# Performance work log

Measured on AMD Instinct MI355X. Metric: run time of the kernel, lower is better.

Reference implementation:

```python
import jax, jax.numpy as jnp
import numpy as np

D = 1024        # inputsize / d_model
G = 8           # groupnum (KV groups)
H = 16          # heads per group
DQ = 128        # qk head dim
DV = 128        # v head dim
FF = 1024       # ffoutsize
B, S = 1, 1024


def _rmsnorm(t, gamma, d_model):
    # torch F.normalize(x, dim=-1) * sqrt(d_model) * gamma
    n = jnp.sqrt(jnp.sum(t * t, axis=-1, keepdims=True))
    return t / jnp.maximum(n, 1e-12) * (d_model ** 0.5) * gamma


def setup_inputs() -> dict:
    key = jax.random.key(0)
    ks = jax.random.split(key, 8)
    std = 0.02
    x = jax.random.normal(ks[0], (B, S, D), dtype=jnp.float32)
    gamma_in = jnp.ones((D,), jnp.float32)
    Wq_w = jax.random.normal(ks[1], (H * G * DQ, D), jnp.float32) * std
    Wq_b = jnp.zeros((H * G * DQ,), jnp.float32)
    Wkv_w = jax.random.normal(ks[2], (G * (DQ + DV), D), jnp.float32) * std
    Wkv_b = jnp.zeros((G * (DQ + DV),), jnp.float32)
    gamma_z = jnp.ones((G * H * DV,), jnp.float32)
    W1 = jax.random.normal(ks[3], (FF * 2, G * H * DV), jnp.float32) * std
    b1 = jnp.zeros((FF * 2,), jnp.float32)
    W2 = jax.random.normal(ks[4], (FF, FF * 2), jnp.float32) * std
    b2 = jnp.zeros((FF,), jnp.float32)
    return {"x": x, "gamma_in": gamma_in, "Wq_w": Wq_w, "Wq_b": Wq_b,
            "Wkv_w": Wkv_w, "Wkv_b": Wkv_b, "gamma_z": gamma_z,
            "W1": W1, "b1": b1, "W2": W2, "b2": b2}


def reference(x, gamma_in, Wq_w, Wq_b, Wkv_w, Wkv_b, gamma_z, W1, b1, W2, b2):
    x = _rmsnorm(x, gamma_in, D)                      # (B,S,D)
    # self-attention path (m is None -> m = x)
    q = (x @ Wq_w.T + Wq_b).reshape(B, S, G, H, DQ)   # (B,S,G,H,dq)
    kv = x @ Wkv_w.T + Wkv_b                          # (B,S,G*(dq+dv))
    k, v = jnp.split(kv, 2, axis=-1)
    k = k.reshape(B, S, G, DQ)                        # (B,S,G,dq)
    v = v.reshape(B, S, G, DV)                        # (B,S,G,dv)
    scale = 1.0 / (DQ ** 0.5)
    scores = jnp.einsum('bsghd,bTgd->bghsT', q, k) * scale  # (B,G,H,S,S)
    attn = jax.nn.softmax(scores, axis=-1)
    z = jnp.einsum('bghsT,bTgd->bsghd', attn, v)      # (B,S,G,H,dv)
    z = z.reshape(B, S, G * H * DV)
    z = _rmsnorm(z, gamma_z, G * H * DV)
    h1 = jax.nn.silu(z @ W1.T + b1)                   # (B,S,2*FF)
    out = jax.nn.silu(h1 @ W2.T + b2)                 # (B,S,FF)
    return out
```

## Files before the change

### kernel.cpp

```cpp
#include <hip/hip_runtime.h>
#include <hip/hip_bf16.h>
#include <math.h>

typedef __attribute__((ext_vector_type(8))) short short8;
typedef __attribute__((ext_vector_type(4))) float floatx4;

__device__ __forceinline__ ushort f2bf(float f) {
  __hip_bfloat16 h = __float2bfloat16(f);
  return *reinterpret_cast<ushort*>(&h);
}
__device__ __forceinline__ float bf2f(ushort u) {
  union { unsigned int i; float f; } c; c.i = ((unsigned)u) << 16; return c.f;
}

__device__ __forceinline__ void lds_dma16(const void* g, void* l) {
  __builtin_amdgcn_global_load_lds((const __attribute__((address_space(1))) void*)g,
                                   (__attribute__((address_space(3))) void*)l, 16, 0, 0);
}

__global__ __launch_bounds__(256) void cvt_all(const float* __restrict__ p0, ushort* __restrict__ o0, int b0,
                                               const float* __restrict__ p1, ushort* __restrict__ o1, int b1,
                                               const float* __restrict__ p2, ushort* __restrict__ o2, int b2,
                                               const float* __restrict__ p3, ushort* __restrict__ o3) {
  int b = blockIdx.x;
  const float* in; ushort* out; int base;
  if (b < b0)            { in = p0; out = o0; base = 0; }
  else if (b < b0 + b1)  { in = p1; out = o1; base = b0; }
  else if (b < b0 + b1 + b2) { in = p2; out = o2; base = b0 + b1; }
  else                   { in = p3; out = o3; base = b0 + b1 + b2; }
  int i = (b - base) * 256 + threadIdx.x;
  float4 v = ((const float4*)in)[i];
  ushort4 o;
  o.x = f2bf(v.x); o.y = f2bf(v.y); o.z = f2bf(v.z); o.w = f2bf(v.w);
  ((ushort4*)out)[i] = o;
}

__global__ __launch_bounds__(256) void rmsnorm_f32(const float* __restrict__ x,
                                                   const float* __restrict__ gamma,
                                                   ushort* __restrict__ y, int D, float sqrtD) {
  const int row = blockIdx.x;
  const float* xr = x + (size_t)row * D;
  float ss = 0.f;
  for (int i = threadIdx.x * 4; i < D; i += 1024) {
    float4 v = *(const float4*)&xr[i];
    ss += v.x * v.x + v.y * v.y + v.z * v.z + v.w * v.w;
  }
#pragma unroll
  for (int off = 1; off < 64; off <<= 1) ss += __shfl_xor(ss, off);
  __shared__ float red[4];
  if ((threadIdx.x & 63) == 0) red[threadIdx.x >> 6] = ss;
  __syncthreads();
  ss = red[0] + red[1] + red[2] + red[3];
  const float sc = sqrtD / fmaxf(sqrtf(ss), 1e-12f);
  for (int i = threadIdx.x * 4; i < D; i += 1024) {
    float4 v = *(const float4*)&xr[i];
    ushort4 o;
    o.x = f2bf(v.x * sc * gamma[i]);
    o.y = f2bf(v.y * sc * gamma[i + 1]);
    o.z = f2bf(v.z * sc * gamma[i + 2]);
    o.w = f2bf(v.w * sc * gamma[i + 3]);
    *(ushort4*)&y[(size_t)row * D + i] = o;
  }
}

__global__ __launch_bounds__(256) void rmsnorm_bf16(const ushort* __restrict__ x,
                                                    const float* __restrict__ gamma,
                                                    ushort* __restrict__ y, int D, float sqrtD) {
  const int row = blockIdx.x;
  const ushort* xr = x + (size_t)row * D;
  float ss = 0.f;
  for (int i = threadIdx.x * 8; i < D; i += 2048) {
    short8 v = *(const short8*)&xr[i];
#pragma unroll
    for (int e = 0; e < 8; e++) { float f = bf2f((ushort)v[e]); ss += f * f; }
  }
#pragma unroll
  for (int off = 1; off < 64; off <<= 1) ss += __shfl_xor(ss, off);
  __shared__ float red[4];
  if ((threadIdx.x & 63) == 0) red[threadIdx.x >> 6] = ss;
  __syncthreads();
  ss = red[0] + red[1] + red[2] + red[3];
  const float sc = sqrtD / fmaxf(sqrtf(ss), 1e-12f);
  for (int i = threadIdx.x * 8; i < D; i += 2048) {
    short8 v = *(const short8*)&xr[i];
    short8 ov;
#pragma unroll
    for (int e = 0; e < 8; e++) ov[e] = (short)f2bf(bf2f((ushort)v[e]) * sc * gamma[i + e]);
    *(short8*)&y[(size_t)row * D + i] = ov;
  }
}

template <int EPI, int ACT, int OUTBF16>
__global__ __launch_bounds__(256, 3) void gemm3(const ushort* __restrict__ A,
                                                const ushort* __restrict__ B,
                                                const float* __restrict__ bias,
                                                const float* __restrict__ bias2,
                                                void* __restrict__ C1,
                                                void* __restrict__ C2,
                                                int M, int N, int K, int Ksplit, float scale) {
  __shared__ ushort As[128 * 64];
  __shared__ ushort Bs[128 * 64];
  const int tid = threadIdx.x;
  const int wave = tid >> 6;
  const int lane = tid & 63;
  const int c16 = lane & 15;
  const int quad = lane >> 4;
  const int wm = wave >> 1;
  const int wn = wave & 1;
  const size_t m0 = (size_t)blockIdx.x * 128;
  const size_t n0 = (size_t)blockIdx.y * 128;
  const int kbeg = blockIdx.z * Ksplit;
  const int kend = kbeg + Ksplit;

  const int rsub = lane >> 3;
  const int csw = (lane & 7) ^ rsub;

  const floatx4 zero = {0.f, 0.f, 0.f, 0.f};
  floatx4 acc[4][4];
#pragma unroll
  for (int a = 0; a < 4; a++)
#pragma unroll
    for (int b = 0; b < 4; b++) acc[a][b] = zero;

  for (int k0 = kbeg; k0 < kend; k0 += 64) {
    __syncthreads();
#pragma unroll
    for (int i = 0; i < 4; i++) {
      const int j = wave * 4 + i;
      const int r = j * 8 + rsub;
      lds_dma16(&A[(m0 + r) * K + k0 + csw * 8], (void*)(As + j * 512));
      lds_dma16(&B[(n0 + r) * K + k0 + csw * 8], (void*)(Bs + j * 512));
    }
    __syncthreads();
#pragma unroll
    for (int kc = 0; kc < 2; kc++) {
      short8 af[4], bf4[4];
#pragma unroll
      for (int mt = 0; mt < 4; mt++) {
        const int row = wm * 64 + mt * 16 + c16;
        af[mt] = *(const short8*)&As[row * 64 + (((kc * 4 + quad) ^ (row & 7)) << 3)];
      }
#pragma unroll
      for (int nt = 0; nt < 4; nt++) {
        const int row = wn * 64 + nt * 16 + c16;
        bf4[nt] = *(const short8*)&Bs[row * 64 + (((kc * 4 + quad) ^ (row & 7)) << 3)];
      }
#pragma unroll
      for (int mt = 0; mt < 4; mt++)
#pragma unroll
        for (int nt = 0; nt < 4; nt++)
          acc[mt][nt] = __builtin_amdgcn_mfma_f32_16x16x32_bf16(af[mt], bf4[nt], acc[mt][nt], 0, 0, 0);
    }
  }

#pragma unroll
  for (int mt = 0; mt < 4; mt++) {
#pragma unroll
    for (int nt = 0; nt < 4; nt++) {
      const size_t col = n0 + wn * 64 + nt * 16 + c16;
      const size_t row0 = m0 + wm * 64 + mt * 16 + quad * 4;
      if (EPI == 0) {
        const float bv = bias[col];
#pragma unroll
        for (int r = 0; r < 4; r++) {
          float v = acc[mt][nt][r] + bv;
          if (ACT) v = v / (1.f + __expf(-v));
          if (OUTBF16) ((ushort*)C1)[(row0 + r) * N + col] = f2bf(v);
          else         ((float*)C1)[(row0 + r) * N + col] = v;
        }
      } else if (EPI == 1) {
        float* plane = (float*)C1 + (size_t)blockIdx.z * M * N;
#pragma unroll
        for (int r = 0; r < 4; r++)
          plane[(row0 + r) * N + col] = acc[mt][nt][r];
      } else {
        if (col < 16384) {
          const float bv = bias[col];
#pragma unroll
          for (int r = 0; r < 4; r++)
            ((ushort*)C1)[(row0 + r) * 16384 + col] = f2bf((acc[mt][nt][r] + bv) * scale);
        } else {
          const size_t ckv = col - 16384;
          const float bv = bias2[ckv];
#pragma unroll
          for (int r = 0; r < 4; r++)
            ((ushort*)C2)[(row0 + r) * 2048 + ckv] = f2bf(acc[mt][nt][r] + bv);
        }
      }
    }
  }
}

template <int NZ, int OUTBF16>
__global__ __launch_bounds__(256) void epi_sum_silu(const float* __restrict__ accb,
                                                    const float* __restrict__ bias,
                                                    void* __restrict__ outp, int N, int n4,
                                                    size_t plane4) {
  int i = blockIdx.x * 256 + threadIdx.x;
  if (i >= n4) return;
  float4 v = ((const float4*)accb)[i];
#pragma unroll
  for (int z = 1; z < NZ; z++) {
    float4 p = ((const float4*)accb)[i + z * plane4];
    v.x += p.x; v.y += p.y; v.z += p.z; v.w += p.w;
  }
  const float4 b = *(const float4*)&bias[(i * 4) % N];
  v.x += b.x; v.y += b.y; v.z += b.z; v.w += b.w;
  v.x = v.x / (1.f + __expf(-v.x));
  v.y = v.y / (1.f + __expf(-v.y));
  v.z = v.z / (1.f + __expf(-v.z));
  v.w = v.w / (1.f + __expf(-v.w));
  if (OUTBF16) {
    ushort4 o; o.x = f2bf(v.x); o.y = f2bf(v.y); o.z = f2bf(v.z); o.w = f2bf(v.w);
    ((ushort4*)outp)[i] = o;
  } else {
    ((float4*)outp)[i] = v;
  }
}

__global__ __launch_bounds__(256) void vtrans(const ushort* __restrict__ KV,
                                              ushort* __restrict__ VT) {
  __shared__ ushort Vl[64 * 138];
  const int tid = threadIdx.x;
  const int t0 = blockIdx.x * 64;
  const int g = blockIdx.y;
#pragma unroll
  for (int i = 0; i < 16; i++) {
    int idx = tid + i * 256;
    int r = idx >> 6, dc = idx & 63;
    *(uint*)&Vl[r * 138 + dc * 2] =
        *(const uint*)&KV[(size_t)(t0 + r) * 2048 + 1024 + g * 128 + dc * 2];
  }
  __syncthreads();
#pragma unroll
  for (int i = 0; i < 4; i++) {
    int idx = tid + i * 256;
    int dv = idx >> 3, tch = idx & 7;
    short8 o;
#pragma unroll
    for (int j = 0; j < 8; j++) o[j] = (short)Vl[(tch * 8 + j) * 138 + dv];
    *(short8*)&VT[(size_t)g * 131072 + (size_t)dv * 1024 + t0 + tch * 8] = o;
  }
}

__global__ __launch_bounds__(256, 2) void attn4(const ushort* __restrict__ Q,
                                                const ushort* __restrict__ KV,
                                                const ushort* __restrict__ VT,
                                                ushort* __restrict__ Z) {
  constexpr int SEQ = 1024;
  __shared__ ushort Kl[64 * 132];
  __shared__ ushort Vt[128 * 68];
  __shared__ ushort Pl[4 * 64 * 68];
  const int tid = threadIdx.x;
  const int wave = tid >> 6;
  const int lane = tid & 63;
  const int c16 = lane & 15;
  const int quad = lane >> 4;
  const int hh = blockIdx.y;
  const int g = hh >> 4;
  const int qbase = blockIdx.x * 256 + wave * 64;
  ushort* Pw = Pl + wave * 64 * 68;

  short8 aq[4][4];
#pragma unroll
  for (int mt = 0; mt < 4; mt++)
#pragma unroll
    for (int kc = 0; kc < 4; kc++)
      aq[mt][kc] = *(const short8*)&Q[(size_t)(qbase + mt * 16 + c16) * 16384 + hh * 128 + kc * 32 + quad * 8];

  const floatx4 zero = {0.f, 0.f, 0.f, 0.f};
  floatx4 o[4][8];
  float lacc[4][4];
#pragma unroll
  for (int mt = 0; mt < 4; mt++) {
#pragma unroll
    for (int nt = 0; nt < 8; nt++) o[mt][nt] = zero;
#pragma unroll
    for (int r = 0; r < 4; r++) lacc[mt][r] = 0.f;
  }

  const ushort* Kg = KV + (size_t)g * 128;
  const ushort* Vg = VT + (size_t)g * 131072;

  for (int t0 = 0; t0 < SEQ; t0 += 64) {
    __syncthreads();
#pragma unroll
    for (int i = 0; i < 4; i++) {
      int idx = tid + i * 256;
      int r = idx >> 4, cc = (idx & 15) << 3;
      *(short8*)&Kl[r * 132 + cc] = *(const short8*)&Kg[(size_t)(t0 + r) * 2048 + cc];
    }
#pragma unroll
    for (int i = 0; i < 4; i++) {
      int idx = tid + i * 256;
      int dv = idx >> 3, ch = (idx & 7) << 3;
      *(short8*)&Vt[dv * 68 + ch] = *(const short8*)&Vg[(size_t)dv * 1024 + t0 + ch];
    }
    __syncthreads();

#pragma unroll
    for (int st = 0; st < 4; st++) {
      floatx4 sacc[4];
#pragma unroll
      for (int mt = 0; mt < 4; mt++) sacc[mt] = zero;
#pragma unroll
      for (int kc = 0; kc < 4; kc++) {
        short8 bk = *(const short8*)&Kl[(st * 16 + c16) * 132 + kc * 32 + quad * 8];
#pragma unroll
        for (int mt = 0; mt < 4; mt++)
          sacc[mt] = __builtin_amdgcn_mfma_f32_16x16x32_bf16(aq[mt][kc], bk, sacc[mt], 0, 0, 0);
      }
#pragma unroll
      for (int mt = 0; mt < 4; mt++) {
#pragma unroll
        for (int r = 0; r < 4; r++) {
          float p = __expf(sacc[mt][r]);
          lacc[mt][r] += p;
          Pw[(mt * 16 + quad * 4 + r) * 68 + st * 16 + c16] = f2bf(p);
        }
      }
    }

#pragma unroll
    for (int tc = 0; tc < 2; tc++) {
      short8 ap[4];
#pragma unroll
      for (int mt = 0; mt < 4; mt++)
        ap[mt] = *(const short8*)&Pw[(mt * 16 + c16) * 68 + tc * 32 + quad * 8];
#pragma unroll
      for (int nt = 0; nt < 8; nt++) {
        short8 bv = *(const short8*)&Vt[(nt * 16 + c16) * 68 + tc * 32 + quad * 8];
#pragma unroll
        for (int mt = 0; mt < 4; mt++)
          o[mt][nt] = __builtin_amdgcn_mfma_f32_16x16x32_bf16(ap[mt], bv, o[mt][nt], 0, 0, 0);
      }
    }
  }

#pragma unroll
  for (int mt = 0; mt < 4; mt++) {
#pragma unroll
    for (int r = 0; r < 4; r++) {
      float l = lacc[mt][r];
      l += __shfl_xor(l, 1);
      l += __shfl_xor(l, 2);
      l += __shfl_xor(l, 4);
      l += __shfl_xor(l, 8);
      float inv = 1.f / l;
      size_t row = (size_t)qbase + mt * 16 + quad * 4 + r;
#pragma unroll
      for (int nt = 0; nt < 8; nt++)
        Z[row * 16384 + hh * 128 + nt * 16 + c16] = f2bf(o[mt][nt][r] * inv);
    }
  }
}

extern "C" void kernel_launch(void* const* d_in, const int* in_sizes, int n_in,
                              void* d_out, int out_size, void* d_ws, size_t ws_size,
                              hipStream_t stream) {
  (void)in_sizes; (void)n_in; (void)out_size; (void)ws_size;
  const float* x        = (const float*)d_in[0];
  const float* gamma_in = (const float*)d_in[1];
  const float* Wq_w     = (const float*)d_in[2];
  const float* Wq_b     = (const float*)d_in[3];
  const float* Wkv_w    = (const float*)d_in[4];
  const float* Wkv_b    = (const float*)d_in[5];
  const float* gamma_z  = (const float*)d_in[6];
  const float* W1       = (const float*)d_in[7];
  const float* b1       = (const float*)d_in[8];
  const float* W2       = (const float*)d_in[9];
  const float* b2       = (const float*)d_in[10];
  float* out = (float*)d_out;

  char* ws = (char*)d_ws;
  size_t off = 0;
  auto alloc = [&](size_t bytes) {
    void* p = ws + off;
    off += (bytes + 255) & ~(size_t)255;
    return p;
  };
  ushort* xn   = (ushort*)alloc((size_t)1024 * 1024 * 2);
  ushort* Wqb  = (ushort*)alloc((size_t)16384 * 1024 * 2);
  ushort* Wkvb = (ushort*)alloc((size_t)2048 * 1024 * 2);
  ushort* W1b  = (ushort*)alloc((size_t)2048 * 16384 * 2);
  ushort* W2b  = (ushort*)alloc((size_t)1024 * 2048 * 2);
  ushort* Qb   = (ushort*)alloc((size_t)1024 * 16384 * 2);
  ushort* KVb  = (ushort*)alloc((size_t)1024 * 2048 * 2);
  ushort* Zb   = Wqb;
  ushort* VTb  = Wkvb;
  ushort* ZN   = Qb;
  float*  h1f  = (float*)Wqb;
  ushort* H1   = Wkvb;
  float*  outf = (float*)Qb;

  cvt_all<<<16384 + 2048 + 32768 + 2048, 256, 0, stream>>>(
      Wq_w, Wqb, 16384, Wkv_w, Wkvb, 2048, W1, W1b, 32768, W2, W2b);

  rmsnorm_f32<<<1024, 256, 0, stream>>>(x, gamma_in, xn, 1024, 32.0f);

  { dim3 g(8, 144, 1);
    gemm3<2, 0, 1><<<g, 256, 0, stream>>>(xn, Wqb, Wq_b, Wkv_b, Qb, KVb,
                                          1024, 18432, 1024, 1024, 0.08838834764831845f); }

  { dim3 g(16, 8); vtrans<<<g, 256, 0, stream>>>(KVb, VTb); }

  { dim3 g(4, 128); attn4<<<g, 256, 0, stream>>>(Qb, KVb, VTb, Zb); }

  rmsnorm_bf16<<<1024, 256, 0, stream>>>(Zb, gamma_z, ZN, 16384, 128.0f);

  { dim3 g(8, 16, 4);
    gemm3<1, 0, 0><<<g, 256, 0, stream>>>(ZN, W1b, b1, nullptr, h1f, nullptr,
                                          1024, 2048, 16384, 4096, 0.f); }
  epi_sum_silu<4, 1><<<2048, 256, 0, stream>>>(h1f, b1, H1, 2048, 1024 * 2048 / 4,
                                               (size_t)1024 * 2048 / 4);

  { dim3 g(8, 8, 4);
    gemm3<1, 0, 0><<<g, 256, 0, stream>>>(H1, W2b, b2, nullptr, outf, nullptr,
                                          1024, 1024, 2048, 512, 0.f); }
  epi_sum_silu<4, 0><<<1024, 256, 0, stream>>>(outf, b2, out, 1024, 1024 * 1024 / 4,
                                               (size_t)1024 * 1024 / 4);
}
```

Measured before the change: 658.0 us.

## Double-buffer attention K/V tiles via async LDS DMA with swizzled layout and 8-wave split

```diff
diff --git a/kernel.cpp b/kernel.cpp
--- a/kernel.cpp
+++ b/kernel.cpp
@@ -243,93 +243,106 @@
   }
 }
 
-__global__ __launch_bounds__(256, 2) void attn4(const ushort* __restrict__ Q,
+__global__ __launch_bounds__(512, 2) void attn6(const ushort* __restrict__ Q,
                                                 const ushort* __restrict__ KV,
                                                 const ushort* __restrict__ VT,
                                                 ushort* __restrict__ Z) {
-  constexpr int SEQ = 1024;
-  __shared__ ushort Kl[64 * 132];
-  __shared__ ushort Vt[128 * 68];
-  __shared__ ushort Pl[4 * 64 * 68];
+  __shared__ ushort Kl[2][64 * 128];
+  __shared__ ushort Vt[2][128 * 64];
+  __shared__ ushort Pl[256 * 68];
+  __shared__ float  Ls[256];
   const int tid = threadIdx.x;
-  const int wave = tid >> 6;
+  const int w = tid >> 6;
   const int lane = tid & 63;
   const int c16 = lane & 15;
   const int quad = lane >> 4;
-  const int hh = blockIdx.y;
+  const int hh = blockIdx.x >> 2;
+  const int qb = blockIdx.x & 3;
   const int g = hh >> 4;
-  const int qbase = blockIdx.x * 256 + wave * 64;
-  ushort* Pw = Pl + wave * 64 * 68;
-
-  short8 aq[4][4];
-#pragma unroll
-  for (int mt = 0; mt < 4; mt++)
-#pragma unroll
-    for (int kc = 0; kc < 4; kc++)
-      aq[mt][kc] = *(const short8*)&Q[(size_t)(qbase + mt * 16 + c16) * 16384 + hh * 128 + kc * 32 + quad * 8];
-
-  const floatx4 zero = {0.f, 0.f, 0.f, 0.f};
-  floatx4 o[4][8];
-  float lacc[4][4];
-#pragma unroll
-  for (int mt = 0; mt < 4; mt++) {
-#pragma unroll
-    for (int nt = 0; nt < 8; nt++) o[mt][nt] = zero;
-#pragma unroll
-    for (int r = 0; r < 4; r++) lacc[mt][r] = 0.f;
-  }
+  const int prow0 = (w & 3) * 64;
+  const int dv0 = (w >> 2) * 64;
 
   const ushort* Kg = KV + (size_t)g * 128;
   const ushort* Vg = VT + (size_t)g * 131072;
 
-  for (int t0 = 0; t0 < SEQ; t0 += 64) {
+  short8 aq[2][4];
+#pragma unroll
+  for (int mt = 0; mt < 2; mt++)
+#pragma unroll
+    for (int kc = 0; kc < 4; kc++)
+      aq[mt][kc] = *(const short8*)&Q[(size_t)(qb * 256 + w * 32 + mt * 16 + c16) * 16384 +
+                                      hh * 128 + kc * 32 + quad * 8];
+
+  const floatx4 zero = {0.f, 0.f, 0.f, 0.f};
+  floatx4 o[4][4];
+  float lacc[2][4];
+#pragma unroll
+  for (int mt = 0; mt < 4; mt++)
+#pragma unroll
+    for (int nt = 0; nt < 4; nt++) o[mt][nt] = zero;
+#pragma unroll
+  for (int mt = 0; mt < 2; mt++)
+#pragma unroll
+    for (int r = 0; r < 4; r++) lacc[mt][r] = 0.f;
+
+  const int kr16 = lane >> 4;
+  const int kc16 = lane & 15;
+  const int vr8 = lane >> 3;
+  const int vc8 = lane & 7;
+
+  auto stage = [&](int buf, int t0) {
+#pragma unroll
+    for (int i = 0; i < 2; i++) {
+      int krow = w * 8 + i * 4 + kr16;
+      int kcs = kc16 ^ (krow & 7);
+      lds_dma16(&Kg[(size_t)(t0 + krow) * 2048 + kcs * 8],
+                (void*)(&Kl[buf][w * 1024 + i * 512]));
+      int vrow = w * 16 + i * 8 + vr8;
+      int vcs = vc8 ^ (vrow & 7);
+      lds_dma16(&Vg[(size_t)vrow * 1024 + t0 + vcs * 8],
+                (void*)(&Vt[buf][w * 1024 + i * 512]));
+    }
+  };
+
+  stage(0, 0);
+
+  for (int t = 0; t < 16; t++) {
+    const int p = t & 1;
     __syncthreads();
-#pragma unroll
-    for (int i = 0; i < 4; i++) {
-      int idx = tid + i * 256;
-      int r = idx >> 4, cc = (idx & 15) << 3;
-      *(short8*)&Kl[r * 132 + cc] = *(const short8*)&Kg[(size_t)(t0 + r) * 2048 + cc];
-    }
-#pragma unroll
-    for (int i = 0; i < 4; i++) {
-      int idx = tid + i * 256;
-      int dv = idx >> 3, ch = (idx & 7) << 3;
-      *(short8*)&Vt[dv * 68 + ch] = *(const short8*)&Vg[(size_t)dv * 1024 + t0 + ch];
+    if (t < 15) stage(p ^ 1, (t + 1) * 64);
+
+#pragma unroll
+    for (int st = 0; st < 4; st++) {
+      floatx4 s0 = zero, s1 = zero;
+      const int krow = st * 16 + c16;
+#pragma unroll
+      for (int kc = 0; kc < 4; kc++) {
+        short8 bk = *(const short8*)&Kl[p][krow * 128 + (((kc * 4 + quad) ^ (c16 & 7)) << 3)];
+        s0 = __builtin_amdgcn_mfma_f32_16x16x32_bf16(aq[0][kc], bk, s0, 0, 0, 0);
+        s1 = __builtin_amdgcn_mfma_f32_16x16x32_bf16(aq[1][kc], bk, s1, 0, 0, 0);
+      }
+#pragma unroll
+      for (int r = 0; r < 4; r++) {
+        float p0 = __expf(s0[r]);
+        float p1 = __expf(s1[r]);
+        lacc[0][r] += p0;
+        lacc[1][r] += p1;
+        Pl[(w * 32 + quad * 4 + r) * 68 + st * 16 + c16] = f2bf(p0);
+        Pl[(w * 32 + 16 + quad * 4 + r) * 68 + st * 16 + c16] = f2bf(p1);
+      }
     }
     __syncthreads();
-
-#pragma unroll
-    for (int st = 0; st < 4; st++) {
-      floatx4 sacc[4];
-#pragma unroll
-      for (int mt = 0; mt < 4; mt++) sacc[mt] = zero;
-#pragma unroll
-      for (int kc = 0; kc < 4; kc++) {
-        short8 bk = *(const short8*)&Kl[(st * 16 + c16) * 132 + kc * 32 + quad * 8];
-#pragma unroll
-        for (int mt = 0; mt < 4; mt++)
-          sacc[mt] = __builtin_amdgcn_mfma_f32_16x16x32_bf16(aq[mt][kc], bk, sacc[mt], 0, 0, 0);
-      }
-#pragma unroll
-      for (int mt = 0; mt < 4; mt++) {
-#pragma unroll
-        for (int r = 0; r < 4; r++) {
-          float p = __expf(sacc[mt][r]);
-          lacc[mt][r] += p;
-          Pw[(mt * 16 + quad * 4 + r) * 68 + st * 16 + c16] = f2bf(p);
-        }
-      }
-    }
 
 #pragma unroll
     for (int tc = 0; tc < 2; tc++) {
       short8 ap[4];
 #pragma unroll
       for (int mt = 0; mt < 4; mt++)
-        ap[mt] = *(const short8*)&Pw[(mt * 16 + c16) * 68 + tc * 32 + quad * 8];
-#pragma unroll
-      for (int nt = 0; nt < 8; nt++) {
-        short8 bv = *(const short8*)&Vt[(nt * 16 + c16) * 68 + tc * 32 + quad * 8];
+        ap[mt] = *(const short8*)&Pl[(prow0 + mt * 16 + c16) * 68 + tc * 32 + quad * 8];
+#pragma unroll
+      for (int nt = 0; nt < 4; nt++) {
+        const int dv = dv0 + nt * 16 + c16;
+        short8 bv = *(const short8*)&Vt[p][dv * 64 + (((tc * 4 + quad) ^ (c16 & 7)) << 3)];
 #pragma unroll
         for (int mt = 0; mt < 4; mt++)
           o[mt][nt] = __builtin_amdgcn_mfma_f32_16x16x32_bf16(ap[mt], bv, o[mt][nt], 0, 0, 0);
@@ -338,7 +351,7 @@
   }
 
 #pragma unroll
-  for (int mt = 0; mt < 4; mt++) {
+  for (int mt = 0; mt < 2; mt++) {
 #pragma unroll
     for (int r = 0; r < 4; r++) {
       float l = lacc[mt][r];
@@ -346,11 +359,20 @@
       l += __shfl_xor(l, 2);
       l += __shfl_xor(l, 4);
       l += __shfl_xor(l, 8);
-      float inv = 1.f / l;
-      size_t row = (size_t)qbase + mt * 16 + quad * 4 + r;
-#pragma unroll
-      for (int nt = 0; nt < 8; nt++)
-        Z[row * 16384 + hh * 128 + nt * 16 + c16] = f2bf(o[mt][nt][r] * inv);
+      if (c16 == 0) Ls[w * 32 + mt * 16 + quad * 4 + r] = l;
+    }
+  }
+  __syncthreads();
+
+#pragma unroll
+  for (int mt = 0; mt < 4; mt++) {
+#pragma unroll
+    for (int r = 0; r < 4; r++) {
+      const float inv = 1.f / Ls[prow0 + mt * 16 + quad * 4 + r];
+      const size_t row = (size_t)qb * 256 + prow0 + mt * 16 + quad * 4 + r;
+#pragma unroll
+      for (int nt = 0; nt < 4; nt++)
+        Z[row * 16384 + hh * 128 + dv0 + nt * 16 + c16] = f2bf(o[mt][nt][r] * inv);
     }
   }
 }
@@ -404,7 +426,7 @@
 
   { dim3 g(16, 8); vtrans<<<g, 256, 0, stream>>>(KVb, VTb); }
 
-  { dim3 g(4, 128); attn4<<<g, 256, 0, stream>>>(Qb, KVb, VTb, Zb); }
+  attn6<<<512, 512, 0, stream>>>(Qb, KVb, VTb, Zb);
 
   rmsnorm_bf16<<<1024, 256, 0, stream>>>(Zb, gamma_z, ZN, 16384, 128.0f);
 
```

Result: faster. 582.7 us (-11.4%).
